# Kernel optimization log

Hardware: AMD Instinct MI355X
Metric: run time of the kernel (lower is better)

Reference implementation:

```python
import jax, jax.numpy as jnp
import numpy as np

N_NODES = 100000
NUM_GRAPHS = 128
HEADS = 4
NEG_SLOPE = 0.2  # PyG GATConv default


def _gat_conv(x, src, dst, W, att_s, att_d, bias, heads, n_nodes, concat):
    # x: [N, F_in]; W: [F_in, heads*C]; att_s/att_d: [heads, C]; bias: [heads*C] or [C]
    h = (x @ W).reshape(n_nodes, heads, -1)            # [N, H, C]
    a_s = jnp.einsum('nhc,hc->nh', h, att_s)            # [N, H]
    a_d = jnp.einsum('nhc,hc->nh', h, att_d)            # [N, H]
    e = jax.nn.leaky_relu(a_s[src] + a_d[dst], NEG_SLOPE)  # [E, H]
    m = jax.ops.segment_max(e, dst, num_segments=n_nodes)  # [N, H]
    ex = jnp.exp(e - m[dst])                                # [E, H]
    denom = jax.ops.segment_sum(ex, dst, num_segments=n_nodes)  # [N, H]
    alpha = ex / (denom[dst] + 1e-16)                       # [E, H]
    msg = h[src] * alpha[:, :, None]                        # [E, H, C]
    out = jax.ops.segment_sum(msg, dst, num_segments=n_nodes)  # [N, H, C]
    if concat:
        out = out.reshape(n_nodes, -1)                      # [N, H*C]
    else:
        out = out.mean(axis=1)                              # [N, C]
    return out + bias


def setup_inputs() -> dict:
    key = jax.random.key(0)
    ks = jax.random.split(key, 12)
    in_c, hid, out_c, H = 128, 32, 10, HEADS
    E = 1600000
    x = jax.random.normal(ks[0], (N_NODES, in_c), dtype=jnp.float32)
    edge_index = jax.random.randint(ks[1], (2, E), 0, N_NODES, dtype=jnp.int32)
    batch = jnp.sort(jax.random.randint(ks[2], (N_NODES,), 0, NUM_GRAPHS, dtype=jnp.int32))
    s1 = 1.0 / np.sqrt(in_c)
    s2 = 1.0 / np.sqrt(hid * H)
    W1 = jax.random.uniform(ks[3], (in_c, H * hid), jnp.float32, -s1, s1)
    att_src1 = jax.random.uniform(ks[4], (H, hid), jnp.float32, -s1, s1)
    att_dst1 = jax.random.uniform(ks[5], (H, hid), jnp.float32, -s1, s1)
    b1 = jnp.zeros((H * hid,), jnp.float32)
    W2 = jax.random.uniform(ks[6], (H * hid, out_c), jnp.float32, -s2, s2)
    att_src2 = jax.random.uniform(ks[7], (1, out_c), jnp.float32, -s2, s2)
    att_dst2 = jax.random.uniform(ks[8], (1, out_c), jnp.float32, -s2, s2)
    b2 = jnp.zeros((out_c,), jnp.float32)
    return {"x": x, "W1": W1, "att_src1": att_src1, "att_dst1": att_dst1, "b1": b1,
            "W2": W2, "att_src2": att_src2, "att_dst2": att_dst2, "b2": b2,
            "edge_index": edge_index, "batch": batch}


def reference(x, W1, att_src1, att_dst1, b1, W2, att_src2, att_dst2, b2, edge_index, batch):
    n = x.shape[0]
    loops = jnp.arange(n, dtype=edge_index.dtype)
    src = jnp.concatenate([edge_index[0], loops])  # add_self_loops=True
    dst = jnp.concatenate([edge_index[1], loops])
    h = jax.nn.elu(_gat_conv(x, src, dst, W1, att_src1, att_dst1, b1, HEADS, n, concat=True))
    h = jax.nn.elu(_gat_conv(h, src, dst, W2, att_src2, att_dst2, b2, 1, n, concat=False))
    # global mean pool over graphs
    sums = jax.ops.segment_sum(h, batch, num_segments=NUM_GRAPHS)
    cnts = jax.ops.segment_sum(jnp.ones((n,), h.dtype), batch, num_segments=NUM_GRAPHS)
    pooled = sums / jnp.maximum(cnts, 1.0)[:, None]
    return jax.nn.log_softmax(pooled, axis=1)
```

## Files before the change

### kernel.cpp

```cpp
#include <hip/hip_runtime.h>
#include <cstdint>
#include <cstddef>

#define LRELU(x) fmaxf((x), 0.2f*(x))

typedef float v2f __attribute__((ext_vector_type(2)));
typedef __attribute__((ext_vector_type(8))) short short8;
typedef __attribute__((ext_vector_type(4))) float f32x4;

__device__ inline unsigned short f2bf(float f) {
  unsigned u = __float_as_uint(f);
  u += 0x8000u;
  return (unsigned short)(u >> 16);
}
__device__ inline float bflo(unsigned u) { return __uint_as_float(u << 16); }
__device__ inline float bfhi(unsigned u) { return __uint_as_float(u & 0xffff0000u); }

__global__ __launch_bounds__(256) void k_gemm1(const float* __restrict__ x,
                                               const float* __restrict__ W1,
                                               const float* __restrict__ atts1,
                                               const float* __restrict__ attd1,
                                               int* __restrict__ h1f8,
                                               float* __restrict__ a_s, float* __restrict__ a_d,
                                               int* __restrict__ deg,
                                               float* __restrict__ poolcnt,
                                               int N) {
  __shared__ short Wt[128*136];
  int t = threadIdx.x;
  int gid = blockIdx.x*256 + t;
  if (gid < N) deg[gid] = 0;
  if (gid < 1408) poolcnt[gid] = 0.f;

  {
    int n = t & 127, half = t >> 7;
    for (int kk0 = 0; kk0 < 64; kk0 += 4) {
      short v0 = (short)f2bf(W1[(half*64 + kk0 + 0)*128 + n]);
      short v1 = (short)f2bf(W1[(half*64 + kk0 + 1)*128 + n]);
      short v2 = (short)f2bf(W1[(half*64 + kk0 + 2)*128 + n]);
      short v3 = (short)f2bf(W1[(half*64 + kk0 + 3)*128 + n]);
      *(short4*)(&Wt[n*136 + half*64 + kk0]) = make_short4(v0, v1, v2, v3);
    }
  }
  __syncthreads();

  int w = t >> 6, l = t & 63;
  int n0 = blockIdx.x*64 + w*16;
  int mrow = l & 15, q = l >> 4;
  int nrow = n0 + mrow; if (nrow >= N) nrow = N - 1;
  const float4* xrow = (const float4*)(x + (size_t)nrow*128);
  f32x4 acc[8];
  #pragma unroll
  for (int i = 0; i < 8; ++i) acc[i] = (f32x4){0.f, 0.f, 0.f, 0.f};
  #pragma unroll
  for (int kc = 0; kc < 4; ++kc) {
    float4 xa = xrow[kc*8 + q*2];
    float4 xb = xrow[kc*8 + q*2 + 1];
    short8 afr;
    afr[0] = (short)f2bf(xa.x); afr[1] = (short)f2bf(xa.y);
    afr[2] = (short)f2bf(xa.z); afr[3] = (short)f2bf(xa.w);
    afr[4] = (short)f2bf(xb.x); afr[5] = (short)f2bf(xb.y);
    afr[6] = (short)f2bf(xb.z); afr[7] = (short)f2bf(xb.w);
    #pragma unroll
    for (int ti = 0; ti < 8; ++ti) {
      short8 bfr = *(const short8*)(&Wt[(ti*16 + mrow)*136 + kc*32 + q*8]);
      acc[ti] = __builtin_amdgcn_mfma_f32_16x16x32_bf16(afr, bfr, acc[ti], 0, 0, 0);
    }
  }
  __syncthreads();
  float* hs = ((float*)Wt) + w*2112;
  #pragma unroll
  for (int ti = 0; ti < 8; ++ti) {
    #pragma unroll
    for (int r = 0; r < 4; ++r)
      hs[(q*4 + r)*132 + ti*16 + mrow] = acc[ti][r];
  }
  {
    int nd = l >> 2, head = l & 3;
    int ndg = n0 + nd;
    const float4* hr  = (const float4*)(hs + nd*132 + head*32);
    const float4* asv = (const float4*)(atts1 + head*32);
    const float4* adv = (const float4*)(attd1 + head*32);
    float ps = 0.f, pd = 0.f;
    int pk[8];
    #pragma unroll
    for (int j = 0; j < 8; ++j) {
      float4 v = hr[j];
      float4 sa = asv[j], da = adv[j];
      ps += v.x*sa.x + v.y*sa.y + v.z*sa.z + v.w*sa.w;
      pd += v.x*da.x + v.y*da.y + v.z*da.z + v.w*da.w;
      int p = __builtin_amdgcn_cvt_pk_fp8_f32(v.x, v.y, 0, false);
      p = __builtin_amdgcn_cvt_pk_fp8_f32(v.z, v.w, p, true);
      pk[j] = p;
    }
    if (ndg < N) {
      int4* dst = (int4*)(h1f8 + (size_t)ndg*32 + head*8);
      dst[0] = make_int4(pk[0], pk[1], pk[2], pk[3]);
      dst[1] = make_int4(pk[4], pk[5], pk[6], pk[7]);
      a_s[ndg*4 + head] = ps;
      a_d[ndg*4 + head] = pd;
    }
  }
}

__global__ __launch_bounds__(256) void k_scatter_f(const int* __restrict__ ei, int E, int Etot,
    int N, int* __restrict__ deg, int* __restrict__ srcs) {
  int b = blockIdx.x;
  int s = b & 7;
  int e = (b >> 3)*256 + threadIdx.x;
  if (e >= Etot) return;
  int dst = (e < E) ? __builtin_nontemporal_load(ei + E + e) : (e - E);
  int lo = (s*N) >> 3;
  int hi = ((s+1)*N) >> 3;
  if (dst < lo || dst >= hi) return;
  int src = (e < E) ? __builtin_nontemporal_load(ei + e) : dst;
  int slot = atomicAdd(&deg[dst], 1);
  if (slot < 64) srcs[(dst << 6) + slot] = src;
}

__global__ __launch_bounds__(256, 8) void k_agg1g2(const int* __restrict__ deg,
    const int* __restrict__ srcs, const float* __restrict__ a_s,
    const float* __restrict__ a_d, const int* __restrict__ h1f8,
    const float* __restrict__ b1, const float* __restrict__ W2,
    const float* __restrict__ atts2, const float* __restrict__ attd2,
    unsigned short* __restrict__ gb, float* __restrict__ a_s2, float* __restrict__ a_d2,
    int N) {
  __shared__ float W2t[1280];
  __shared__ float att2s[20];
  int t = threadIdx.x;
  for (int f = t; f < 1280; f += 256) {
    int c = f >> 7, k = f & 127;
    W2t[f] = W2[k*10 + c];
  }
  if (t < 20) att2s[t] = (t < 10) ? atts2[t] : attd2[t - 10];
  __syncthreads();

  int dst = (blockIdx.x*256 + t) >> 5;
  if (dst >= N) return;
  int l = t & 31;
  int sub = l & 15;
  int epair = l >> 4;
  int myhead = sub >> 2;
  int eh = l & 3;
  int ee = l >> 2;
  int beg = dst << 6;
  int dcnt = deg[dst]; if (dcnt > 64) dcnt = 64;
  int end = beg + dcnt;
  float4 ad4 = ((const float4*)a_d)[dst];
  float adh = (eh==0) ? ad4.x : (eh==1) ? ad4.y : (eh==2) ? ad4.z : ad4.w;
  float wacc = 0.f;
  v2f accA = (v2f){0.f,0.f}, accB = (v2f){0.f,0.f};
  v2f accC = (v2f){0.f,0.f}, accD = (v2f){0.f,0.f};
  const float4* as4p = (const float4*)a_s;
  const int2* h2p = (const int2*)h1f8;

  for (int g = beg; g < end; g += 32) {
    int gl = g + l;
    int se_all = srcs[gl < end ? gl : end - 1];
    int sec0 = __shfl(se_all, 0*8 + ee, 32);
    int sec1 = __shfl(se_all, 1*8 + ee, 32);
    int sec2 = __shfl(se_all, 2*8 + ee, 32);
    int sec3 = __shfl(se_all, 3*8 + ee, 32);
    float4 g0 = as4p[sec0];
    float4 g1 = as4p[sec1];
    float4 g2 = as4p[sec2];
    float4 g3 = as4p[sec3];
    float ash0 = (eh==0) ? g0.x : (eh==1) ? g0.y : (eh==2) ? g0.z : g0.w;
    float ash1 = (eh==0) ? g1.x : (eh==1) ? g1.y : (eh==2) ? g1.z : g1.w;
    float ash2 = (eh==0) ? g2.x : (eh==1) ? g2.y : (eh==2) ? g2.z : g2.w;
    float ash3 = (eh==0) ? g3.x : (eh==1) ? g3.y : (eh==2) ? g3.z : g3.w;
    float ashs[4] = {ash0, ash1, ash2, ash3};
    int nrem = end - g;
    #pragma unroll
    for (int c = 0; c < 4; ++c) {
      if (c*8 >= nrem) break;
      int rm = nrem - c*8 - 1;
      float w = __expf(LRELU(ashs[c] + adh));
      if (ee > rm) w = 0.f;
      wacc += w;
      int2 u[4]; float we[4];
      #pragma unroll
      for (int k = 0; k < 4; ++k) {
        int e = k*2 + epair;
        int s_e = __shfl(se_all, c*8 + e, 32);
        we[k]   = __shfl(w, e*4 + myhead, 32);
        u[k] = h2p[(size_t)s_e*16 + sub];
      }
      #pragma unroll
      for (int k = 0; k < 4; ++k) {
        v2f lo0 = __builtin_amdgcn_cvt_pk_f32_fp8(u[k].x, false);
        v2f hi0 = __builtin_amdgcn_cvt_pk_f32_fp8(u[k].x, true);
        v2f lo1 = __builtin_amdgcn_cvt_pk_f32_fp8(u[k].y, false);
        v2f hi1 = __builtin_amdgcn_cvt_pk_f32_fp8(u[k].y, true);
        v2f wv = (v2f){we[k], we[k]};
        accA += wv*lo0; accB += wv*hi0; accC += wv*lo1; accD += wv*hi1;
      }
    }
  }
  wacc += __shfl_xor(wacc, 4, 32);
  wacc += __shfl_xor(wacc, 8, 32);
  wacc += __shfl_xor(wacc, 16, 32);
  float denom = __shfl(wacc, myhead, 32);

  accA.x += __shfl_xor(accA.x, 16, 32); accA.y += __shfl_xor(accA.y, 16, 32);
  accB.x += __shfl_xor(accB.x, 16, 32); accB.y += __shfl_xor(accB.y, 16, 32);
  accC.x += __shfl_xor(accC.x, 16, 32); accC.y += __shfl_xor(accC.y, 16, 32);
  accD.x += __shfl_xor(accD.x, 16, 32); accD.y += __shfl_xor(accD.y, 16, 32);

  float inv = 1.0f / (denom + 1e-16f);
  float4 b1a = ((const float4*)b1)[sub*2];
  float4 b1b = ((const float4*)b1)[sub*2 + 1];
  float h0 = accA.x*inv + b1a.x; h0 = h0 > 0.f ? h0 : __expf(h0) - 1.0f;
  float h1 = accA.y*inv + b1a.y; h1 = h1 > 0.f ? h1 : __expf(h1) - 1.0f;
  float h2 = accB.x*inv + b1a.z; h2 = h2 > 0.f ? h2 : __expf(h2) - 1.0f;
  float h3 = accB.y*inv + b1a.w; h3 = h3 > 0.f ? h3 : __expf(h3) - 1.0f;
  float h4 = accC.x*inv + b1b.x; h4 = h4 > 0.f ? h4 : __expf(h4) - 1.0f;
  float h5 = accC.y*inv + b1b.y; h5 = h5 > 0.f ? h5 : __expf(h5) - 1.0f;
  float h6 = accD.x*inv + b1b.z; h6 = h6 > 0.f ? h6 : __expf(h6) - 1.0f;
  float h7 = accD.y*inv + b1b.w; h7 = h7 > 0.f ? h7 : __expf(h7) - 1.0f;

  const float4* W2t4 = (const float4*)W2t;
  float pc[5];
  #pragma unroll
  for (int cq = 0; cq < 5; ++cq) {
    int c = epair*5 + cq;
    float4 w0 = W2t4[c*32 + sub*2];
    float4 w1 = W2t4[c*32 + sub*2 + 1];
    pc[cq] = h0*w0.x + h1*w0.y + h2*w0.z + h3*w0.w
           + h4*w1.x + h5*w1.y + h6*w1.z + h7*w1.w;
  }
  #pragma unroll
  for (int off = 8; off > 0; off >>= 1) {
    #pragma unroll
    for (int cq = 0; cq < 5; ++cq)
      pc[cq] += __shfl_xor(pc[cq], off, 32);
  }
  if (sub < 5) {
    float val = pc[0];
    #pragma unroll
    for (int cq = 1; cq < 5; ++cq) val = (sub == cq) ? pc[cq] : val;
    gb[(size_t)dst*16 + epair*5 + sub] = f2bf(val);
  }
  float asH = 0.f, advH = 0.f;
  #pragma unroll
  for (int cq = 0; cq < 5; ++cq) {
    asH  += pc[cq]*att2s[epair*5 + cq];
    advH += pc[cq]*att2s[10 + epair*5 + cq];
  }
  asH  += __shfl_xor(asH, 16, 32);
  advH += __shfl_xor(advH, 16, 32);
  if (l == 0) {
    a_s2[dst] = asH;
    a_d2[dst] = advH;
  }
}

__global__ __launch_bounds__(256) void k_agg2f(const int* __restrict__ deg,
    const int* __restrict__ srcs, const float* __restrict__ a_s,
    const float* __restrict__ a_d, const unsigned short* __restrict__ gb,
    const float* __restrict__ b2, const int* __restrict__ batch,
    float* __restrict__ pooled, float* __restrict__ cnt, int N) {
  __shared__ float lp[4*10];
  __shared__ float lc[4];
  __shared__ int b0s;
  int t = threadIdx.x;
  int dst = (blockIdx.x*256 + t) >> 4;
  int l = t & 15;
  if (t < 40) lp[t] = 0.f;
  if (t < 4) lc[t] = 0.f;
  if (t == 0) {
    int d0 = (blockIdx.x*256) >> 4;
    if (d0 > N - 1) d0 = N - 1;
    b0s = batch[d0];
  }
  __syncthreads();
  int b0 = b0s;
  bool valid = (dst < N);
  float o = 0.f;
  int b = 0;
  if (valid) {
    int beg = dst << 6;
    int dcnt = deg[dst]; if (dcnt > 64) dcnt = 64;
    int end = beg + dcnt;
    float ad = a_d[dst];
    float acc[10] = {};
    float denom = 0.f;
    const uint4* g4 = (const uint4*)gb;
    const unsigned* gu = (const unsigned*)gb;
    int j = beg + l;
    if (j < end) {
      int s0 = srcs[j];
      int j1 = j + 16;
      int s1 = (j1 < end) ? srcs[j1] : s0;
      float av0 = a_s[s0];
      uint4  A0 = g4[(size_t)s0*2];
      unsigned B0 = gu[(size_t)s0*8 + 4];
      for (; j < end; j += 16) {
        float av1 = a_s[s1];
        uint4  A1 = g4[(size_t)s1*2];
        unsigned B1 = gu[(size_t)s1*8 + 4];
        int j2 = j + 32;
        int s2 = (j2 < end) ? srcs[j2] : s1;
        float w = __expf(LRELU(av0 + ad));
        denom += w;
        acc[0] += w*bflo(A0.x); acc[1] += w*bfhi(A0.x);
        acc[2] += w*bflo(A0.y); acc[3] += w*bfhi(A0.y);
        acc[4] += w*bflo(A0.z); acc[5] += w*bfhi(A0.z);
        acc[6] += w*bflo(A0.w); acc[7] += w*bfhi(A0.w);
        acc[8] += w*bflo(B0);   acc[9] += w*bfhi(B0);
        av0 = av1; A0 = A1; B0 = B1; s1 = s2;
      }
    }
    #pragma unroll
    for (int off = 8; off > 0; off >>= 1) {
      denom += __shfl_xor(denom, off, 16);
      #pragma unroll
      for (int c = 0; c < 10; ++c) acc[c] += __shfl_xor(acc[c], off, 16);
    }
    b = batch[dst];
    if (l < 10) {
      o = acc[l] / (denom + 1e-16f) + b2[l];
      o = o > 0.f ? o : __expf(o) - 1.0f;
    }
  }
  if (valid) {
    int bl = b - b0;
    if (l < 10) {
      if (bl < 4) atomicAdd(&lp[bl*10 + l], o);
      else atomicAdd(&pooled[b*10 + l], o);
    }
    if (l == 0) {
      if (bl < 4) atomicAdd(&lc[bl], 1.0f);
      else atomicAdd(&cnt[b], 1.0f);
    }
  }
  __syncthreads();
  if (t < 40) {
    int bl = t / 10, c = t - bl*10;
    int bb = b0 + bl;
    if (bb < 128 && lp[t] != 0.f) atomicAdd(&pooled[bb*10 + c], lp[t]);
  }
  if (t < 4) {
    int bb = b0 + t;
    if (bb < 128 && lc[t] != 0.f) atomicAdd(&cnt[bb], lc[t]);
  }
}

__global__ __launch_bounds__(128) void k_softmax(const float* __restrict__ pooled,
    const float* __restrict__ cnt, float* __restrict__ out) {
  int t = threadIdx.x;
  float inv = 1.0f / fmaxf(cnt[t], 1.0f);
  float v[10], m = -1e30f;
  #pragma unroll
  for (int c = 0; c < 10; ++c) { v[c] = pooled[t*10 + c] * inv; m = fmaxf(m, v[c]); }
  float s = 0.f;
  #pragma unroll
  for (int c = 0; c < 10; ++c) s += __expf(v[c] - m);
  float ls = logf(s) + m;
  #pragma unroll
  for (int c = 0; c < 10; ++c) out[t*10 + c] = v[c] - ls;
}

extern "C" void kernel_launch(void* const* d_in, const int* in_sizes, int n_in,
                              void* d_out, int out_size, void* d_ws, size_t ws_size,
                              hipStream_t stream) {
  const float* x     = (const float*)d_in[0];
  const float* W1    = (const float*)d_in[1];
  const float* atts1 = (const float*)d_in[2];
  const float* attd1 = (const float*)d_in[3];
  const float* b1    = (const float*)d_in[4];
  const float* W2    = (const float*)d_in[5];
  const float* atts2 = (const float*)d_in[6];
  const float* attd2 = (const float*)d_in[7];
  const float* b2    = (const float*)d_in[8];
  const int*   ei    = (const int*)d_in[9];
  const int*   batch = (const int*)d_in[10];
  int N = in_sizes[10];
  int E = in_sizes[9] / 2;
  int Etot = E + N;

  char* base = (char*)d_ws;
  size_t off = 0;
  auto allocB = [&](size_t bytes) { void* p = (void*)(base + off); off += (bytes + 63) & ~size_t(63); return p; };

  int*   h1f8   = (int*)allocB((size_t)N*32*sizeof(int));
  float* a_s1   = (float*)allocB((size_t)N*4*sizeof(float));
  float* a_d1   = (float*)allocB((size_t)N*4*sizeof(float));
  unsigned short* gb = (unsigned short*)allocB((size_t)N*16*sizeof(unsigned short));
  float* a_s2   = (float*)allocB((size_t)N*sizeof(float));
  float* a_d2   = (float*)allocB((size_t)N*sizeof(float));
  float* poolcnt= (float*)allocB(1408*sizeof(float));
  int* deg    = (int*)allocB((size_t)N*sizeof(int));
  int* srcs   = (int*)allocB((size_t)N*64*sizeof(int));

  float* pooled = poolcnt;
  float* cnt    = poolcnt + 1280;
  int tilesE = (Etot + 255) / 256;

  k_gemm1<<<dim3((N + 63)/64), dim3(256), 0, stream>>>(x, W1, atts1, attd1, h1f8,
                                                       a_s1, a_d1, deg, poolcnt, N);
  k_scatter_f<<<dim3(tilesE*8), dim3(256), 0, stream>>>(ei, E, Etot, N, deg, srcs);
  k_agg1g2<<<dim3((N*32 + 255)/256), dim3(256), 0, stream>>>(deg, srcs, a_s1, a_d1, h1f8,
                                                             b1, W2, atts2, attd2,
                                                             gb, a_s2, a_d2, N);
  k_agg2f<<<dim3((N*16 + 255)/256), dim3(256), 0, stream>>>(deg, srcs, a_s2, a_d2, gb,
                                                            b2, batch, pooled, cnt, N);
  k_softmax<<<dim3(1), dim3(128), 0, stream>>>(pooled, cnt, (float*)d_out);
}
```

Baseline: 310.5 us.

## Replace global-atomic edge scatter with two-phase bucket partition and LDS counting

The previous CSR build read the edge list eight times and did a global atomicAdd on per-node degree counters. It is replaced by two kernels. The first partitions edges into 64 destination-range buckets using a shared-memory histogram and one global atomic per bucket per block. The second gives each bucket one block that counts per-node slots with LDS atomics and writes degrees directly. This removes the repeated edge reads and the contended global atomics. In exchange it adds a 13.6 MB intermediate buffer, and the second pass runs only 64 blocks, which may underuse the GPU.

```diff
diff --git a/kernel.cpp b/kernel.cpp
--- a/kernel.cpp
+++ b/kernel.cpp
@@ -22,13 +22,13 @@
                                                const float* __restrict__ attd1,
                                                int* __restrict__ h1f8,
                                                float* __restrict__ a_s, float* __restrict__ a_d,
-                                               int* __restrict__ deg,
+                                               int* __restrict__ bcnt,
                                                float* __restrict__ poolcnt,
                                                int N) {
   __shared__ short Wt[128*136];
   int t = threadIdx.x;
   int gid = blockIdx.x*256 + t;
-  if (gid < N) deg[gid] = 0;
+  if (gid < 64) bcnt[gid] = 0;
   if (gid < 1408) poolcnt[gid] = 0.f;
 
   {
@@ -102,19 +102,58 @@
   }
 }
 
-__global__ __launch_bounds__(256) void k_scatter_f(const int* __restrict__ ei, int E, int Etot,
-    int N, int* __restrict__ deg, int* __restrict__ srcs) {
-  int b = blockIdx.x;
-  int s = b & 7;
-  int e = (b >> 3)*256 + threadIdx.x;
-  if (e >= Etot) return;
-  int dst = (e < E) ? __builtin_nontemporal_load(ei + E + e) : (e - E);
-  int lo = (s*N) >> 3;
-  int hi = ((s+1)*N) >> 3;
-  if (dst < lo || dst >= hi) return;
-  int src = (e < E) ? __builtin_nontemporal_load(ei + e) : dst;
-  int slot = atomicAdd(&deg[dst], 1);
-  if (slot < 64) srcs[(dst << 6) + slot] = src;
+__global__ __launch_bounds__(256) void k_part(const int* __restrict__ ei, int E, int Etot,
+    int Nd, int cap, int* __restrict__ bcnt, int2* __restrict__ bdata) {
+  __shared__ int hist[64];
+  __shared__ int cur[64];
+  int t = threadIdx.x;
+  if (t < 64) hist[t] = 0;
+  __syncthreads();
+  int base = blockIdx.x*4096;
+  int dreg[16]; signed char sreg[16];
+  #pragma unroll
+  for (int k = 0; k < 16; ++k) {
+    int e = base + k*256 + t;
+    int s = -1, d = 0;
+    if (e < Etot) {
+      d = (e < E) ? ei[E + e] : (e - E);
+      s = d / Nd;
+      atomicAdd(&hist[s], 1);
+    }
+    dreg[k] = d; sreg[k] = (signed char)s;
+  }
+  __syncthreads();
+  if (t < 64) cur[t] = atomicAdd(&bcnt[t], hist[t]);
+  __syncthreads();
+  #pragma unroll
+  for (int k = 0; k < 16; ++k) {
+    int s = sreg[k];
+    if (s < 0) continue;
+    int e = base + k*256 + t;
+    int src = (e < E) ? ei[e] : dreg[k];
+    int pos = atomicAdd(&cur[s], 1);
+    if (pos < cap) bdata[(size_t)s*cap + pos] = make_int2(src, dreg[k]);
+  }
+}
+
+__global__ __launch_bounds__(256) void k_scatter_b(const int2* __restrict__ bdata,
+    const int* __restrict__ bcnt, int Nd, int cap, int N,
+    int* __restrict__ deg, int* __restrict__ srcs) {
+  __shared__ int lcnt[2560];
+  int t = threadIdx.x;
+  int s = blockIdx.x;
+  int lo = s*Nd;
+  for (int i = t; i < Nd; i += 256) lcnt[i] = 0;
+  __syncthreads();
+  int cnt = bcnt[s]; if (cnt > cap) cnt = cap;
+  const int2* bp = bdata + (size_t)s*cap;
+  for (int i = t; i < cnt; i += 256) {
+    int2 ev = bp[i];
+    int slot = atomicAdd(&lcnt[ev.y - lo], 1);
+    if (slot < 64) srcs[((size_t)ev.y << 6) + slot] = ev.x;
+  }
+  __syncthreads();
+  for (int i = t; i < Nd && lo + i < N; i += 256) deg[lo + i] = lcnt[i];
 }
 
 __global__ __launch_bounds__(256, 8) void k_agg1g2(const int* __restrict__ deg,
@@ -377,6 +416,8 @@
   int N = in_sizes[10];
   int E = in_sizes[9] / 2;
   int Etot = E + N;
+  int Nd  = (N + 63) / 64;
+  int cap = (Etot >> 6) + 4096;
 
   char* base = (char*)d_ws;
   size_t off = 0;
@@ -389,16 +430,19 @@
   float* a_s2   = (float*)allocB((size_t)N*sizeof(float));
   float* a_d2   = (float*)allocB((size_t)N*sizeof(float));
   float* poolcnt= (float*)allocB(1408*sizeof(float));
+  int* bcnt   = (int*)allocB(64*sizeof(int));
   int* deg    = (int*)allocB((size_t)N*sizeof(int));
   int* srcs   = (int*)allocB((size_t)N*64*sizeof(int));
+  int2* bdata = (int2*)allocB((size_t)64*cap*sizeof(int2));
 
   float* pooled = poolcnt;
   float* cnt    = poolcnt + 1280;
-  int tilesE = (Etot + 255) / 256;
+  int nblkA = (Etot + 4095) / 4096;
 
   k_gemm1<<<dim3((N + 63)/64), dim3(256), 0, stream>>>(x, W1, atts1, attd1, h1f8,
-                                                       a_s1, a_d1, deg, poolcnt, N);
-  k_scatter_f<<<dim3(tilesE*8), dim3(256), 0, stream>>>(ei, E, Etot, N, deg, srcs);
+                                                       a_s1, a_d1, bcnt, poolcnt, N);
+  k_part<<<dim3(nblkA), dim3(256), 0, stream>>>(ei, E, Etot, Nd, cap, bcnt, bdata);
+  k_scatter_b<<<dim3(64), dim3(256), 0, stream>>>(bdata, bcnt, Nd, cap, N, deg, srcs);
   k_agg1g2<<<dim3((N*32 + 255)/256), dim3(256), 0, stream>>>(deg, srcs, a_s1, a_d1, h1f8,
                                                              b1, W2, atts2, attd2,
                                                              gb, a_s2, a_d2, N);
```

After: 309.3 us. No clear change (-0.4%).
